# Kernel tuning notes

Measured on AMD Instinct MI355X. Metric: run time of the kernel, lower is better.

The kernel has to match this reference:

```python
import jax, jax.numpy as jnp
import numpy as np

EMBED, HEADS, LEVELS, POINTS, MLP = 256, 8, 3, 4, 4
SHAPES = [(60, 80), (30, 40), (15, 20)]  # (H, W) per level


def layer_norm(x, g, b):
    m = jnp.mean(x, -1, keepdims=True)
    v = jnp.mean((x - m) ** 2, -1, keepdims=True)
    return (x - m) * jax.lax.rsqrt(v + 1e-5) * g + b


def _bilinear(v, H, W, gx, gy):
    # v: [B,h,H*W,dh]; gx,gy: [B,h,Nq,P] absolute pixel coords (grid_sample align_corners=False, zero padding)
    x0 = jnp.floor(gx); y0 = jnp.floor(gy)
    wx = gx - x0; wy = gy - y0

    def g(xi, yi):
        valid = ((xi >= 0) & (xi < W) & (yi >= 0) & (yi < H)).astype(v.dtype)
        idx = jnp.clip(yi, 0, H - 1) * W + jnp.clip(xi, 0, W - 1)
        B, h, Nq, P = idx.shape
        out = jnp.take_along_axis(v, idx.reshape(B, h, Nq * P)[..., None], axis=2)
        return out.reshape(B, h, Nq, P, -1) * valid[..., None]

    x0i = x0.astype(jnp.int32); y0i = y0.astype(jnp.int32)
    return (g(x0i, y0i) * ((1 - wx) * (1 - wy))[..., None]
            + g(x0i + 1, y0i) * (wx * (1 - wy))[..., None]
            + g(x0i, y0i + 1) * ((1 - wx) * wy)[..., None]
            + g(x0i + 1, y0i + 1) * (wx * wy)[..., None])


def setup_inputs() -> dict:
    key = jax.random.key(0)
    ks = jax.random.split(key, 16)
    B, Nq, C = 2, 8192, EMBED
    Nv = sum(h * w for h, w in SHAPES)
    s = 0.02
    d = {
        'query': jax.random.normal(ks[0], (B, Nq, C), jnp.float32),
        'value': jax.random.normal(ks[1], (B, Nv, C), jnp.float32),
        'query_pos': jax.random.normal(ks[2], (B, Nq, C), jnp.float32),
        'ref_pts': jax.random.uniform(ks[3], (B, Nq, LEVELS, 2), jnp.float32),
        'spatial_shapes': jnp.array(SHAPES, jnp.int32),
        'level_start_index': jnp.array(np.cumsum([0] + [h * w for h, w in SHAPES[:-1]]), jnp.int32),
        'g1': jnp.ones((C,), jnp.float32), 'b1': jnp.zeros((C,), jnp.float32),
        'Wo': s * jax.random.normal(ks[4], (C, HEADS * LEVELS * POINTS * 2), jnp.float32),
        'bo': jnp.zeros((HEADS * LEVELS * POINTS * 2,), jnp.float32),
        'Wa': s * jax.random.normal(ks[5], (C, HEADS * LEVELS * POINTS), jnp.float32),
        'ba': jnp.zeros((HEADS * LEVELS * POINTS,), jnp.float32),
        'Wv': s * jax.random.normal(ks[6], (C, C), jnp.float32), 'bv': jnp.zeros((C,), jnp.float32),
        'Wp': s * jax.random.normal(ks[7], (C, C), jnp.float32), 'bp': jnp.zeros((C,), jnp.float32),
        'g2': jnp.ones((C,), jnp.float32), 'b2': jnp.zeros((C,), jnp.float32),
        'Wf1': s * jax.random.normal(ks[8], (C, MLP * C), jnp.float32), 'bf1': jnp.zeros((MLP * C,), jnp.float32),
        'Wf2': s * jax.random.normal(ks[9], (MLP * C, C), jnp.float32), 'bf2': jnp.zeros((C,), jnp.float32),
    }
    return d


def reference(query, value, query_pos, ref_pts, spatial_shapes, level_start_index,
              g1, b1, Wo, bo, Wa, ba, Wv, bv, Wp, bp, g2, b2, Wf1, bf1, Wf2, bf2):
    B, Nq, C = query.shape
    dh = C // HEADS
    shapes = np.asarray(spatial_shapes).tolist()
    starts = np.asarray(level_start_index).tolist()

    qn = layer_norm(query, g1, b1)           # pre-norm
    qa = qn + query_pos                       # positional embedding inside attn
    offs = (qa @ Wo + bo).reshape(B, Nq, HEADS, LEVELS, POINTS, 2)
    aw = jax.nn.softmax((qa @ Wa + ba).reshape(B, Nq, HEADS, LEVELS * POINTS), -1)
    aw = aw.reshape(B, Nq, HEADS, LEVELS, POINTS)
    v = (value @ Wv + bv).reshape(B, -1, HEADS, dh).transpose(0, 2, 1, 3)  # [B,h,Nv,dh]

    # offset_normalizer = (W, H) per level
    norm = jnp.array([[w, h] for h, w in shapes], jnp.float32)
    loc = ref_pts[:, :, None, :, None, :] + offs / norm[None, None, None, :, None, :]

    out = jnp.zeros((B, Nq, HEADS, dh), query.dtype)
    for l, (H, W) in enumerate(shapes):
        vl = jax.lax.dynamic_slice_in_dim(v, starts[l], H * W, axis=2)
        gl = loc[:, :, :, l].transpose(0, 2, 1, 3, 4)   # [B,h,Nq,P,2]
        gx = gl[..., 0] * W - 0.5
        gy = gl[..., 1] * H - 0.5
        sampled = _bilinear(vl, H, W, gx, gy)            # [B,h,Nq,P,dh]
        out = out + jnp.einsum('bhqpd,bqhp->bqhd', sampled, aw[:, :, :, l])

    attn = out.reshape(B, Nq, C) @ Wp + bp + qn          # output proj + mmcv internal residual (identity=norm1(query))
    q = query + attn                                     # layer residual
    q2 = layer_norm(q, g2, b2)
    return q + (jax.nn.gelu(q2 @ Wf1 + bf1, approximate=False) @ Wf2 + bf2)
```

## Files before the change

kernel.cpp:

```cpp
#include <hip/hip_runtime.h>
#include <math.h>


typedef short short8 __attribute__((ext_vector_type(8)));
typedef short s16x4 __attribute__((ext_vector_type(4)));
typedef __bf16 bf16x8 __attribute__((ext_vector_type(8)));
typedef float f32x4 __attribute__((ext_vector_type(4)));

#if defined(__has_attribute)
#if __has_attribute(amdgpu_num_vgpr)
#define WPMLP_REGS __attribute__((amdgpu_num_vgpr(128)))
#else
#define WPMLP_REGS
#endif
#else
#define WPMLP_REGS
#endif

__device__ __forceinline__ short f2b(float f) {
  unsigned u = __builtin_bit_cast(unsigned, f);
  u += 0x7fffu + ((u >> 16) & 1u);
  return (short)(u >> 16);
}
__device__ __forceinline__ float b2f(short s) {
  unsigned u = ((unsigned)(unsigned short)s) << 16;
  return __builtin_bit_cast(float, u);
}
__device__ __forceinline__ void b8f(short8 s, float* f) {
  const uint4 u = __builtin_bit_cast(uint4, s);
  f[0] = __builtin_bit_cast(float, u.x << 16);
  f[1] = __builtin_bit_cast(float, u.x & 0xffff0000u);
  f[2] = __builtin_bit_cast(float, u.y << 16);
  f[3] = __builtin_bit_cast(float, u.y & 0xffff0000u);
  f[4] = __builtin_bit_cast(float, u.z << 16);
  f[5] = __builtin_bit_cast(float, u.z & 0xffff0000u);
  f[6] = __builtin_bit_cast(float, u.w << 16);
  f[7] = __builtin_bit_cast(float, u.w & 0xffff0000u);
}

__device__ __forceinline__ f32x4 mfma16(short8 a, short8 b, f32x4 c) {
  return __builtin_amdgcn_mfma_f32_16x16x32_bf16(
      __builtin_bit_cast(bf16x8, a), __builtin_bit_cast(bf16x8, b), c, 0, 0, 0);
}

typedef __attribute__((address_space(3))) unsigned int lds_u32;
typedef const __attribute__((address_space(1))) unsigned int glb_u32;
__device__ __forceinline__ void glds16(const void* g, void* l) {
  __builtin_amdgcn_global_load_lds((glb_u32*)g, (lds_u32*)l, 16, 0, 0);
}

__device__ __forceinline__ float gelu1(float v) {
  return 0.5f * v * (1.f + erff(v * 0.70710678118654752f));
}

template <int EPI>
__device__ __forceinline__ void gemm64_core(
    int bx, int by,
    const short* __restrict__ A, const short* __restrict__ Bt,
    const float* __restrict__ bias, const float* __restrict__ bias2,
    void* __restrict__ Cout, int M, int Nreal, int ldc, int K, char* smem)
{
  short* sA = (short*)smem;
  short* sB = sA + 4096;
  float* sf = (float*)smem;

  const int t = threadIdx.x;
  const int wave = t >> 6, lane = t & 63;
  const int quad = lane >> 4, l16 = lane & 15;
  const int wm = (wave & 1) * 32, wn = (wave >> 1) * 64;
  const int m0 = by * 64, n0 = bx * 128;

  f32x4 acc[2][4];
#pragma unroll
  for (int i = 0; i < 2; i++)
#pragma unroll
    for (int j = 0; j < 4; j++) acc[i][j] = (f32x4){0.f, 0.f, 0.f, 0.f};

  const int srow = lane >> 3, pos = lane & 7;
  const int chunk = (pos + srow) & 7;
  const short* gA = A + (size_t)(m0 + wave * 16 + srow) * K + chunk * 8;
  const short* gB = Bt + (size_t)(n0 + wave * 32 + srow) * K + chunk * 8;

  const int nk = K >> 6;
  for (int kt = 0; kt < nk; ++kt) {
    if (kt) __syncthreads();
    const int ko = kt * 64;
#pragma unroll
    for (int g = 0; g < 2; ++g)
      glds16(gA + ko + (size_t)(g * 8) * K, sA + (wave * 16 + g * 8) * 64);
#pragma unroll
    for (int g = 0; g < 4; ++g)
      glds16(gB + ko + (size_t)(g * 8) * K, sB + (wave * 32 + g * 8) * 64);
    __syncthreads();
#pragma unroll
    for (int kk = 0; kk < 2; ++kk) {
      short8 af[2], bf[4];
      const int c = kk * 4 + quad;
#pragma unroll
      for (int i = 0; i < 2; i++) {
        const int lrA = wm + i * 16 + l16;
        af[i] = *(const short8*)&sA[lrA * 64 + ((c - lrA) & 7) * 8];
      }
#pragma unroll
      for (int j = 0; j < 4; j++) {
        const int lrB = wn + j * 16 + l16;
        bf[j] = *(const short8*)&sB[lrB * 64 + ((c - lrB) & 7) * 8];
      }
#pragma unroll
      for (int i = 0; i < 2; i++)
#pragma unroll
        for (int j = 0; j < 4; j++) acc[i][j] = mfma16(bf[j], af[i], acc[i][j]);
    }
  }
  __syncthreads();

#pragma unroll
  for (int b = 0; b < 2; ++b) {
    if (wm == b * 32) {
#pragma unroll
      for (int i = 0; i < 2; ++i) {
        const int rr = i * 16 + l16;
#pragma unroll
        for (int j = 0; j < 4; ++j)
          *(f32x4*)&sf[rr * 132 + wn + quad * 4 + j * 16] = acc[i][j];
      }
    }
    __syncthreads();
#pragma unroll
    for (int r2 = 0; r2 < 4; ++r2) {
      const int fidx = r2 * 1024 + t * 4;
      const int row = fidx >> 7, col = fidx & 127;
      const int gm = m0 + b * 32 + row;
      const int cc = n0 + col;
      if (gm < M && cc < Nreal) {
        const float4 v = *(const float4*)&sf[row * 132 + col];
        float4 bb;
        if (EPI == 4) bb = (cc < 192) ? *(const float4*)(bias + cc)
                                      : *(const float4*)(bias2 + cc - 192);
        else bb = *(const float4*)(bias + cc);
        float v0 = v.x + bb.x, v1 = v.y + bb.y, v2 = v.z + bb.z, v3 = v.w + bb.w;
        s16x4 o; o.x = f2b(v0); o.y = f2b(v1); o.z = f2b(v2); o.w = f2b(v3);
        *(s16x4*)((short*)Cout + (size_t)gm * ldc + cc) = o;
      }
    }
    __syncthreads();
  }
}

__global__ __launch_bounds__(256) void gemm_oa_v(
    const short* __restrict__ qa, const short* __restrict__ wt_oa,
    const float* __restrict__ bo, const float* __restrict__ ba,
    short* __restrict__ oabuf,
    const short* __restrict__ valbf, const short* __restrict__ wt_v,
    const float* __restrict__ bv, short* __restrict__ vproj)
{
  __shared__ __align__(16) char smem[24576];
  const int idx = blockIdx.x;
  if (idx < 768) {
    gemm64_core<4>(idx % 3, idx / 3, qa, wt_oa, bo, ba,
                   oabuf, 16384, 288, 288, 256, smem);
  } else {
    const int r = idx - 768;
    gemm64_core<5>(r % 2, r / 2, valbf, wt_v, bv, nullptr,
                   vproj, 12600, 256, 256, 256, smem);
  }
}

__global__ __launch_bounds__(512) WPMLP_REGS void wp_mlp(
    const short* __restrict__ sampled,
    const short* __restrict__ wtp,
    const float* __restrict__ bp,
    const short* __restrict__ qnb,
    const float* __restrict__ query,
    const float* __restrict__ g2, const float* __restrict__ b2v,
    const short* __restrict__ wf1,
    const float* __restrict__ b1v,
    const short* __restrict__ wf2,
    const float* __restrict__ bf2v,
    float* __restrict__ outp)
{
  __shared__ __align__(16) char smem[81920];
  float* Q  = (float*)smem;
  short* H  = (short*)(smem + 32768);
  float* QY = (float*)(smem + 32768);
  short* RA = (short*)(smem + 65536);

  const int t = threadIdx.x;
  const int w = t >> 6, lane = t & 63;
  const int quad = lane >> 4, l16 = lane & 15;
  const int wm2 = w >> 2, wn4 = w & 3;
  const int m0 = blockIdx.x * 32;

#pragma unroll
  for (int q = 0; q < 2; ++q) {
    const int g = q * 512 + t;
    const int row = g >> 5, p = g & 31;
    const int cl = (p & ~7) | ((p + row) & 7);
    glds16(sampled + (size_t)(m0 + row) * 256 + cl * 8,
           RA + (q * 512 + w * 64) * 8);
  }
#pragma unroll
  for (int q = 0; q < 4; ++q) {
    const int g = q * 512 + t;
    glds16(query + (size_t)(m0 + (g >> 6)) * 256 + (g & 63) * 4,
           QY + (q * 512 + w * 64) * 4);
  }
  __syncthreads();

  {
    f32x4 accp[4];
#pragma unroll
    for (int j = 0; j < 4; j++) accp[j] = (f32x4){0.f, 0.f, 0.f, 0.f};
#pragma unroll
    for (int kk = 0; kk < 8; ++kk) {
      const int c = kk * 4 + quad;
      const int r = wm2 * 16 + l16;
      const int pos = (c & ~7) | ((c - r) & 7);
      const short8 afr = *(const short8*)(RA + r * 256 + pos * 8);
      short8 bfr[4];
#pragma unroll
      for (int j = 0; j < 4; ++j) {
        const int n1 = wn4 * 4 + j;
        bfr[j] = *(const short8*)(wtp + ((size_t)n1 * 32 + c) * 128 + l16 * 8);
      }
#pragma unroll
      for (int j = 0; j < 4; ++j) accp[j] = mfma16(bfr[j], afr, accp[j]);
    }
#pragma unroll
    for (int j = 0; j < 4; ++j) {
      const int r = wm2 * 16 + l16;
      const int c = wn4 * 64 + j * 16 + quad * 4;
      *(f32x4*)&Q[r * 256 + (c ^ ((r & 7) << 2))] = accp[j];
    }
  }
  __syncthreads();

  {
    const float4 bbp  = *(const float4*)(bp + lane * 4);
    const float4 gv   = *(const float4*)(g2 + lane * 4);
    const float4 bb2  = *(const float4*)(b2v + lane * 4);
#pragma unroll
    for (int rep = 0; rep < 4; ++rep) {
      const int row = rep * 8 + w;
      const int gm = m0 + row;
      const int cs = (lane * 4) ^ ((row & 7) << 2);
      const float4 a  = *(const float4*)&Q[row * 256 + cs];
      const float4 qv = *(const float4*)&QY[row * 256 + lane * 4];
      const s16x4 qn  = *(const s16x4*)(qnb + (size_t)gm * 256 + lane * 4);
      float v0 = a.x + bbp.x + b2f(qn.x) + qv.x;
      float v1 = a.y + bbp.y + b2f(qn.y) + qv.y;
      float v2 = a.z + bbp.z + b2f(qn.z) + qv.z;
      float v3 = a.w + bbp.w + b2f(qn.w) + qv.w;
      float s = v0 + v1 + v2 + v3;
#pragma unroll
      for (int o = 32; o; o >>= 1) s += __shfl_xor(s, o);
      const float mean = s * (1.f / 256.f);
      const float d0 = v0 - mean, d1 = v1 - mean, d2 = v2 - mean, d3 = v3 - mean;
      float ss = d0 * d0 + d1 * d1 + d2 * d2 + d3 * d3;
#pragma unroll
      for (int o = 32; o; o >>= 1) ss += __shfl_xor(ss, o);
      const float inv = rsqrtf(ss * (1.f / 256.f) + 1e-5f);
      *(f32x4*)&Q[row * 256 + cs] = (f32x4){v0, v1, v2, v3};
      const int col = lane * 4;
      const int c = col >> 3;
      const int pos = (c & ~7) | ((c - row) & 7);
      s16x4 o2;
      o2.x = f2b(d0 * inv * gv.x + bb2.x);
      o2.y = f2b(d1 * inv * gv.y + bb2.y);
      o2.z = f2b(d2 * inv * gv.z + bb2.z);
      o2.w = f2b(d3 * inv * gv.w + bb2.w);
      *(s16x4*)(RA + row * 256 + pos * 8 + (col & 7)) = o2;
    }
  }
  __syncthreads();

  f32x4 acc2[4];
#pragma unroll
  for (int j = 0; j < 4; j++) acc2[j] = (f32x4){0.f, 0.f, 0.f, 0.f};

  for (int h = 0; h < 2; ++h) {
    if (h) __syncthreads();
    f32x4 acc1[8];
#pragma unroll
    for (int j = 0; j < 8; j++) acc1[j] = (f32x4){0.f, 0.f, 0.f, 0.f};
#pragma unroll
    for (int kk = 0; kk < 8; ++kk) {
      const int cg = kk * 4 + quad;
      const int r = wm2 * 16 + l16;
      const int pos = (cg & ~7) | ((cg - r) & 7);
      const short8 afr = *(const short8*)(RA + r * 256 + pos * 8);
      short8 bfr[8];
#pragma unroll
      for (int j = 0; j < 8; ++j) {
        const int n1 = h * 32 + wn4 * 8 + j;
        bfr[j] = *(const short8*)(wf1 + ((size_t)n1 * 32 + cg) * 128 + l16 * 8);
      }
#pragma unroll
      for (int j = 0; j < 8; ++j) acc1[j] = mfma16(bfr[j], afr, acc1[j]);
    }
#pragma unroll
    for (int j = 0; j < 8; ++j) {
      const int coll = wn4 * 128 + j * 16 + quad * 4;
      const float4 bb = *(const float4*)(b1v + h * 512 + coll);
      const int c = coll >> 3;
      const int r = wm2 * 16 + l16;
      const int pos = (c & ~7) | ((c - r) & 7);
      s16x4 o;
      o.x = f2b(gelu1(acc1[j].x + bb.x));
      o.y = f2b(gelu1(acc1[j].y + bb.y));
      o.z = f2b(gelu1(acc1[j].z + bb.z));
      o.w = f2b(gelu1(acc1[j].w + bb.w));
      *(s16x4*)(H + r * 512 + pos * 8 + (coll & 7)) = o;
    }
    __syncthreads();

#pragma unroll 4
    for (int kk = 0; kk < 16; ++kk) {
      const int cl = kk * 4 + quad;
      const int r = wm2 * 16 + l16;
      const int pos = (cl & ~7) | ((cl - r) & 7);
      const short8 afr = *(const short8*)(H + r * 512 + pos * 8);
      short8 bfr[4];
#pragma unroll
      for (int j = 0; j < 4; ++j) {
        const int n1 = wn4 * 4 + j;
        bfr[j] = *(const short8*)(wf2 + ((size_t)n1 * 128 + h * 64 + cl) * 128 + l16 * 8);
      }
#pragma unroll
      for (int j = 0; j < 4; ++j) acc2[j] = mfma16(bfr[j], afr, acc2[j]);
    }
  }
  __syncthreads();

#pragma unroll
  for (int j = 0; j < 4; ++j) {
    const int r = wm2 * 16 + l16;
    const int c = wn4 * 64 + j * 16 + quad * 4;
    *(f32x4*)&QY[r * 256 + (c ^ ((r & 7) << 2))] = acc2[j];
  }
  __syncthreads();

  {
    const float4 bbf = *(const float4*)(bf2v + lane * 4);
#pragma unroll
    for (int rep = 0; rep < 4; ++rep) {
      const int row = rep * 8 + w;
      const int gm = m0 + row;
      const int cs = (lane * 4) ^ ((row & 7) << 2);
      const float4 v  = *(const float4*)&QY[row * 256 + cs];
      const float4 qb = *(const float4*)&Q[row * 256 + cs];
      *(float4*)(outp + (size_t)gm * 256 + lane * 4) =
          make_float4(v.x + bbf.x + qb.x, v.y + bbf.y + qb.y,
                      v.z + bbf.z + qb.z, v.w + bbf.w + qb.w);
    }
  }
}

__global__ __launch_bounds__(256) void prep_all(
    const float* __restrict__ Wo, const float* __restrict__ Wa,
    const float* __restrict__ Wv, const float* __restrict__ Wp,
    const float* __restrict__ Wf1, const float* __restrict__ Wf2,
    short* __restrict__ t_oa, short* __restrict__ t_v, short* __restrict__ t_p,
    short* __restrict__ t_f1, short* __restrict__ t_f2,
    const float* __restrict__ value, short* __restrict__ valbf,
    const float* __restrict__ query, const float* __restrict__ query_pos,
    const float* __restrict__ g1, const float* __restrict__ b1,
    short* __restrict__ qnb, short* __restrict__ qa)
{
  __shared__ float tile[32][33];
  const int t = threadIdx.x;
  const int blk = blockIdx.x;

  if (blk < 1792) {
    const int bxa = blk & 255, bya = blk >> 8;
    int K, N, noff; const float* src; short* dst;
    switch (bya) {
      case 0: src = Wo;      dst = t_oa; K = 256;  N = 192;  noff = 0;   break;
      case 1: src = Wa;      dst = t_oa; K = 256;  N = 96;   noff = 192; break;
      case 2: src = nullptr; dst = t_oa; K = 256;  N = 96;   noff = 288; break;
      case 3: src = Wv;      dst = t_v;  K = 256;  N = 256;  noff = 0;   break;
      case 4: src = Wp;      dst = t_p;  K = 256;  N = 256;  noff = 0;   break;
      case 5: src = Wf1;     dst = t_f1; K = 256;  N = 1024; noff = 0;   break;
      default: src = Wf2;    dst = t_f2; K = 1024; N = 256;  noff = 0;   break;
    }
    const bool fragpack = (bya >= 4);
    const int tilesK = K >> 5;
    const int nt = tilesK * (N >> 5);
    if (bxa >= nt) return;
    const int tk = bxa % tilesK, tn = bxa / tilesK;
    const int k0 = tk * 32, n0 = tn * 32;
    const int r = t >> 3, c4 = (t & 7) * 4;
    float4 v = make_float4(0.f, 0.f, 0.f, 0.f);
    if (src) v = *(const float4*)(src + (size_t)(k0 + r) * N + n0 + c4);
    tile[r][c4] = v.x; tile[r][c4 + 1] = v.y; tile[r][c4 + 2] = v.z; tile[r][c4 + 3] = v.w;
    __syncthreads();
    const int nn = t >> 3, kc = (t & 7) * 4;
    s16x4 o;
    o.x = f2b(tile[kc][nn]); o.y = f2b(tile[kc + 1][nn]);
    o.z = f2b(tile[kc + 2][nn]); o.w = f2b(tile[kc + 3][nn]);
    if (fragpack) {
      const int n = n0 + nn, k = k0 + kc;
      *(s16x4*)(dst + ((size_t)(n >> 4) * (K >> 3) + (k >> 3)) * 128 +
                (n & 15) * 8 + (k & 7)) = o;
    } else {
      *(s16x4*)(dst + (size_t)(noff + n0 + nn) * K + k0 + kc) = o;
    }
  } else if (blk < 1792 + 3169) {
    const int i = ((blk - 1792) * 256 + t) * 4;
    if (i >= 12672 * 256) return;
    s16x4 o = (s16x4){0, 0, 0, 0};
    if (i < 12600 * 256) {
      float4 v = *(const float4*)(value + i);
      o.x = f2b(v.x); o.y = f2b(v.y); o.z = f2b(v.z); o.w = f2b(v.w);
    }
    *(s16x4*)(valbf + i) = o;
  } else {
    const int row  = (blk - 4961) * 4 + (t >> 6);
    const int lane = t & 63;
    const float4 v = ((const float4*)(query + (size_t)row * 256))[lane];
    float s = v.x + v.y + v.z + v.w;
#pragma unroll
    for (int o = 32; o; o >>= 1) s += __shfl_xor(s, o);
    const float mean = s * (1.f / 256.f);
    const float dx = v.x - mean, dy = v.y - mean, dz = v.z - mean, dw = v.w - mean;
    float s2 = dx * dx + dy * dy + dz * dz + dw * dw;
#pragma unroll
    for (int o = 32; o; o >>= 1) s2 += __shfl_xor(s2, o);
    const float inv = rsqrtf(s2 * (1.f / 256.f) + 1e-5f);
    const float4 gv = ((const float4*)g1)[lane];
    const float4 bv = ((const float4*)b1)[lane];
    const float4 o1 = make_float4(dx * inv * gv.x + bv.x, dy * inv * gv.y + bv.y,
                                  dz * inv * gv.z + bv.z, dw * inv * gv.w + bv.w);
    s16x4 ob; ob.x = f2b(o1.x); ob.y = f2b(o1.y); ob.z = f2b(o1.z); ob.w = f2b(o1.w);
    ((s16x4*)(qnb + (size_t)row * 256))[lane] = ob;
    const float4 pv = ((const float4*)(query_pos + (size_t)row * 256))[lane];
    s16x4 op;
    op.x = f2b(o1.x + pv.x); op.y = f2b(o1.y + pv.y);
    op.z = f2b(o1.z + pv.z); op.w = f2b(o1.w + pv.w);
    ((s16x4*)(qa + (size_t)row * 256))[lane] = op;
  }
}

__global__ __launch_bounds__(256) void deform_fused(
    const short* __restrict__ vproj, const short* __restrict__ oa,
    const float* __restrict__ refp, short* __restrict__ out)
{
  __shared__ int4 sIdx[768];
  __shared__ s16x4 sW[768];
  const int t = threadIdx.x;

  if (t < 64) {
    const int row = blockIdx.x * 8 + (t >> 3), h = t & 7;
    const short* oarow = oa + (size_t)row * 288;
    float off[24];
    {
      const short8* op = (const short8*)(oarow + h * 24);
      b8f(op[0], off); b8f(op[1], off + 8); b8f(op[2], off + 16);
    }
    float lg[12];
    {
      const s16x4* ap = (const s16x4*)(oarow + 192 + h * 12);
#pragma unroll
      for (int i = 0; i < 3; i++) {
        const s16x4 v = ap[i];
        lg[i * 4] = b2f(v.x); lg[i * 4 + 1] = b2f(v.y);
        lg[i * 4 + 2] = b2f(v.z); lg[i * 4 + 3] = b2f(v.w);
      }
    }
    const float* rp = refp + (size_t)row * 6;
    const float Rx[3] = {rp[0], rp[2], rp[4]}, Ry[3] = {rp[1], rp[3], rp[5]};
    float mx = lg[0];
#pragma unroll
    for (int i = 1; i < 12; i++) mx = fmaxf(mx, lg[i]);
    float sum = 0.f;
#pragma unroll
    for (int i = 0; i < 12; i++) { lg[i] = __expf(lg[i] - mx); sum += lg[i]; }
    const float inv = 1.f / sum;
    const int b = row >> 13;
    const int Hs[3] = {60, 30, 15}, Ws[3] = {80, 40, 20}, St[3] = {0, 4800, 6000};
#pragma unroll
    for (int p = 0; p < 12; p++) {
      const int l = p >> 2;
      const int W = Ws[l], H = Hs[l];
      const float gx = Rx[l] * W + off[p * 2]     - 0.5f;
      const float gy = Ry[l] * H + off[p * 2 + 1] - 0.5f;
      const float x0f = floorf(gx), y0f = floorf(gy);
      const float wx = gx - x0f, wy = gy - y0f;
      const int x0 = (int)x0f, y0 = (int)y0f;
      const float aw = lg[p] * inv;
      float cw[4] = {(1.f - wx) * (1.f - wy), wx * (1.f - wy),
                     (1.f - wx) * wy, wx * wy};
      const int base = b * 6300 + St[l];
      int ci[4];
#pragma unroll
      for (int k = 0; k < 4; k++) {
        const int xx = x0 + (k & 1), yy = y0 + (k >> 1);
        const bool valid = (xx >= 0) & (xx < W) & (yy >= 0) & (yy < H);
        const int xc = min(max(xx, 0), W - 1);
        const int yc = min(max(yy, 0), H - 1);
        ci[k] = ((base + yc * W + xc) << 8) + h * 32;
        cw[k] = valid ? cw[k] * aw : 0.f;
      }
      sIdx[t * 12 + p] = make_int4(ci[0], ci[1], ci[2], ci[3]);
      s16x4 wv; wv.x = f2b(cw[0]); wv.y = f2b(cw[1]); wv.z = f2b(cw[2]); wv.w = f2b(cw[3]);
      sW[t * 12 + p] = wv;
    }
  }
  __syncthreads();

  const int lu = t >> 2, c4 = (t & 3) * 8;
  float acc[8];
#pragma unroll
  for (int i = 0; i < 8; i++) acc[i] = 0.f;
#pragma unroll 2
  for (int p = 0; p < 12; p++) {
    const int4 idx = sIdx[lu * 12 + p];
    const s16x4 wb = sW[lu * 12 + p];
    const float w0 = b2f(wb.x), w1 = b2f(wb.y), w2 = b2f(wb.z), w3 = b2f(wb.w);
    const short8 v0 = *(const short8*)(vproj + idx.x + c4);
    const short8 v1 = *(const short8*)(vproj + idx.y + c4);
    const short8 v2 = *(const short8*)(vproj + idx.z + c4);
    const short8 v3 = *(const short8*)(vproj + idx.w + c4);
    float f0[8], f1[8], f2[8], f3[8];
    b8f(v0, f0); b8f(v1, f1); b8f(v2, f2); b8f(v3, f3);
#pragma unroll
    for (int j = 0; j < 8; j++)
      acc[j] += w0 * f0[j] + w1 * f1[j] + w2 * f2[j] + w3 * f3[j];
  }
  short8 o;
#pragma unroll
  for (int j = 0; j < 8; j++) o[j] = f2b(acc[j]);
  *(short8*)(out + (size_t)(blockIdx.x * 256 + t) * 8) = o;
}

extern "C" void kernel_launch(void* const* d_in, const int* in_sizes, int n_in,
                              void* d_out, int out_size, void* d_ws, size_t ws_size,
                              hipStream_t stream)
{
  const float* query     = (const float*)d_in[0];
  const float* value     = (const float*)d_in[1];
  const float* query_pos = (const float*)d_in[2];
  const float* ref_pts   = (const float*)d_in[3];
  const float* g1  = (const float*)d_in[6];
  const float* b1  = (const float*)d_in[7];
  const float* Wo  = (const float*)d_in[8];
  const float* bo  = (const float*)d_in[9];
  const float* Wa  = (const float*)d_in[10];
  const float* ba  = (const float*)d_in[11];
  const float* Wv  = (const float*)d_in[12];
  const float* bv  = (const float*)d_in[13];
  const float* Wp  = (const float*)d_in[14];
  const float* bp  = (const float*)d_in[15];
  const float* g2  = (const float*)d_in[16];
  const float* b2  = (const float*)d_in[17];
  const float* Wf1 = (const float*)d_in[18];
  const float* bf1 = (const float*)d_in[19];
  const float* Wf2 = (const float*)d_in[20];
  const float* bf2 = (const float*)d_in[21];

  char* ws = (char*)d_ws;
  short* wt_oa   = (short*)(ws + 0);
  short* wt_v    = (short*)(ws + 196608);
  short* wt_p    = (short*)(ws + 327680);
  short* wt_f1   = (short*)(ws + 458752);
  short* wt_f2   = (short*)(ws + 983040);
  short* qnb     = (short*)(ws + 1507328);
  short* qa      = (short*)(ws + 18284544);
  short* oabuf   = (short*)(ws + 26673152);
  short* vproj   = (short*)(ws + 45547520);
  short* sampled = (short*)(ws + 51998720);
  short* valbf   = (short*)(ws + 77164544);
  float* outp = (float*)d_out;

  prep_all<<<9057, 256, 0, stream>>>(Wo, Wa, Wv, Wp, Wf1, Wf2,
                                     wt_oa, wt_v, wt_p, wt_f1, wt_f2,
                                     value, valbf, query, query_pos,
                                     g1, b1, qnb, qa);
  gemm_oa_v<<<1162, 256, 0, stream>>>(qa, wt_oa, bo, ba, oabuf,
                                      valbf, wt_v, bv, vproj);
  deform_fused<<<2048, 256, 0, stream>>>(vproj, oabuf, ref_pts, sampled);
  wp_mlp<<<512, 512, 0, stream>>>(sampled, wt_p, bp, qnb, query, g2, b2,
                                  wt_f1, bf1, wt_f2, bf2, outp);
}
```

Before: 248.8 us.

## Shrink wp_mlp LDS to 64KB by chunking hidden dim into four 256-wide slices

The fused output-projection/MLP kernel now processes the 1024-wide hidden layer in four 256-column chunks instead of two 512-column chunks. This halves the H staging buffer, halves the acc1 register footprint, and removes the QY buffer. The query residual is read directly from global memory, and the final bias plus residual is accumulated in registers into Q before a single store pass. Shared memory drops from 80KB to 64KB, which may let more blocks fit per CU, at the cost of extra barriers per block and an uncached global read of query.

```diff
diff --git a/kernel.cpp b/kernel.cpp
--- a/kernel.cpp
+++ b/kernel.cpp
@@ -179,11 +179,10 @@
     const float* __restrict__ bf2v,
     float* __restrict__ outp)
 {
-  __shared__ __align__(16) char smem[81920];
+  __shared__ __align__(16) char smem[65536];
   float* Q  = (float*)smem;
   short* H  = (short*)(smem + 32768);
-  float* QY = (float*)(smem + 32768);
-  short* RA = (short*)(smem + 65536);
+  short* RA = (short*)(smem + 49152);
 
   const int t = threadIdx.x;
   const int w = t >> 6, lane = t & 63;
@@ -199,12 +198,6 @@
     glds16(sampled + (size_t)(m0 + row) * 256 + cl * 8,
            RA + (q * 512 + w * 64) * 8);
   }
-#pragma unroll
-  for (int q = 0; q < 4; ++q) {
-    const int g = q * 512 + t;
-    glds16(query + (size_t)(m0 + (g >> 6)) * 256 + (g & 63) * 4,
-           QY + (q * 512 + w * 64) * 4);
-  }
   __syncthreads();
 
   {
@@ -245,7 +238,7 @@
       const int gm = m0 + row;
       const int cs = (lane * 4) ^ ((row & 7) << 2);
       const float4 a  = *(const float4*)&Q[row * 256 + cs];
-      const float4 qv = *(const float4*)&QY[row * 256 + lane * 4];
+      const float4 qv = *(const float4*)(query + (size_t)gm * 256 + lane * 4);
       const s16x4 qn  = *(const s16x4*)(qnb + (size_t)gm * 256 + lane * 4);
       float v0 = a.x + bbp.x + b2f(qn.x) + qv.x;
       float v1 = a.y + bbp.y + b2f(qn.y) + qv.y;
@@ -278,30 +271,30 @@
 #pragma unroll
   for (int j = 0; j < 4; j++) acc2[j] = (f32x4){0.f, 0.f, 0.f, 0.f};
 
-  for (int h = 0; h < 2; ++h) {
-    if (h) __syncthreads();
-    f32x4 acc1[8];
-#pragma unroll
-    for (int j = 0; j < 8; j++) acc1[j] = (f32x4){0.f, 0.f, 0.f, 0.f};
+  for (int q = 0; q < 4; ++q) {
+    if (q) __syncthreads();
+    f32x4 acc1[4];
+#pragma unroll
+    for (int j = 0; j < 4; j++) acc1[j] = (f32x4){0.f, 0.f, 0.f, 0.f};
 #pragma unroll
     for (int kk = 0; kk < 8; ++kk) {
       const int cg = kk * 4 + quad;
       const int r = wm2 * 16 + l16;
       const int pos = (cg & ~7) | ((cg - r) & 7);
       const short8 afr = *(const short8*)(RA + r * 256 + pos * 8);
-      short8 bfr[8];
-#pragma unroll
-      for (int j = 0; j < 8; ++j) {
-        const int n1 = h * 32 + wn4 * 8 + j;
+      short8 bfr[4];
+#pragma unroll
+      for (int j = 0; j < 4; ++j) {
+        const int n1 = q * 16 + wn4 * 4 + j;
         bfr[j] = *(const short8*)(wf1 + ((size_t)n1 * 32 + cg) * 128 + l16 * 8);
       }
 #pragma unroll
-      for (int j = 0; j < 8; ++j) acc1[j] = mfma16(bfr[j], afr, acc1[j]);
-    }
-#pragma unroll
-    for (int j = 0; j < 8; ++j) {
-      const int coll = wn4 * 128 + j * 16 + quad * 4;
-      const float4 bb = *(const float4*)(b1v + h * 512 + coll);
+      for (int j = 0; j < 4; ++j) acc1[j] = mfma16(bfr[j], afr, acc1[j]);
+    }
+#pragma unroll
+    for (int j = 0; j < 4; ++j) {
+      const int coll = wn4 * 64 + j * 16 + quad * 4;
+      const float4 bb = *(const float4*)(b1v + q * 256 + coll);
       const int c = coll >> 3;
       const int r = wm2 * 16 + l16;
       const int pos = (c & ~7) | ((c - r) & 7);
@@ -310,49 +303,49 @@
       o.y = f2b(gelu1(acc1[j].y + bb.y));
       o.z = f2b(gelu1(acc1[j].z + bb.z));
       o.w = f2b(gelu1(acc1[j].w + bb.w));
-      *(s16x4*)(H + r * 512 + pos * 8 + (coll & 7)) = o;
+      *(s16x4*)(H + r * 256 + pos * 8 + (coll & 7)) = o;
     }
     __syncthreads();
 
 #pragma unroll 4
-    for (int kk = 0; kk < 16; ++kk) {
+    for (int kk = 0; kk < 8; ++kk) {
       const int cl = kk * 4 + quad;
       const int r = wm2 * 16 + l16;
       const int pos = (cl & ~7) | ((cl - r) & 7);
-      const short8 afr = *(const short8*)(H + r * 512 + pos * 8);
+      const short8 afr = *(const short8*)(H + r * 256 + pos * 8);
       short8 bfr[4];
 #pragma unroll
       for (int j = 0; j < 4; ++j) {
         const int n1 = wn4 * 4 + j;
-        bfr[j] = *(const short8*)(wf2 + ((size_t)n1 * 128 + h * 64 + cl) * 128 + l16 * 8);
+        bfr[j] = *(const short8*)(wf2 + ((size_t)n1 * 128 + q * 32 + cl) * 128 + l16 * 8);
       }
 #pragma unroll
       for (int j = 0; j < 4; ++j) acc2[j] = mfma16(bfr[j], afr, acc2[j]);
     }
   }
+
+  {
+#pragma unroll
+    for (int j = 0; j < 4; ++j) {
+      const int r = wm2 * 16 + l16;
+      const int c = wn4 * 64 + j * 16 + quad * 4;
+      const int cs = c ^ ((r & 7) << 2);
+      const float4 bb = *(const float4*)(bf2v + c);
+      const float4 qb = *(const float4*)&Q[r * 256 + cs];
+      *(f32x4*)&Q[r * 256 + cs] =
+          (f32x4){qb.x + acc2[j].x + bb.x, qb.y + acc2[j].y + bb.y,
+                  qb.z + acc2[j].z + bb.z, qb.w + acc2[j].w + bb.w};
+    }
+  }
   __syncthreads();
 
 #pragma unroll
-  for (int j = 0; j < 4; ++j) {
-    const int r = wm2 * 16 + l16;
-    const int c = wn4 * 64 + j * 16 + quad * 4;
-    *(f32x4*)&QY[r * 256 + (c ^ ((r & 7) << 2))] = acc2[j];
-  }
-  __syncthreads();
-
-  {
-    const float4 bbf = *(const float4*)(bf2v + lane * 4);
-#pragma unroll
-    for (int rep = 0; rep < 4; ++rep) {
-      const int row = rep * 8 + w;
-      const int gm = m0 + row;
-      const int cs = (lane * 4) ^ ((row & 7) << 2);
-      const float4 v  = *(const float4*)&QY[row * 256 + cs];
-      const float4 qb = *(const float4*)&Q[row * 256 + cs];
-      *(float4*)(outp + (size_t)gm * 256 + lane * 4) =
-          make_float4(v.x + bbf.x + qb.x, v.y + bbf.y + qb.y,
-                      v.z + bbf.z + qb.z, v.w + bbf.w + qb.w);
-    }
+  for (int rep = 0; rep < 4; ++rep) {
+    const int row = rep * 8 + w;
+    const int gm = m0 + row;
+    const int cs = (lane * 4) ^ ((row & 7) << 2);
+    const float4 v = *(const float4*)&Q[row * 256 + cs];
+    *(float4*)(outp + (size_t)gm * 256 + lane * 4) = v;
   }
 }
 
```

Measured after the change: 219.6 us. 11.7% less time.
